# Kernel tuning notes

Measured on AMD Instinct MI355X. Metric: run time of the kernel, lower is better.

Reference implementation:

```python
import jax, jax.numpy as jnp
import numpy as np

B, S, D, H = 2, 2048, 1024, 16
HD = D // H  # head_dim = 64


def setup_inputs() -> dict:
    key = jax.random.key(0)
    ks = jax.random.split(key, 9)
    xav = float(np.sqrt(6.0 / (D + D)))  # xavier_uniform bound for square matrices
    def lin_w(k):
        return jax.random.uniform(k, (D, D), jnp.float32, -xav, xav)
    return {
        "x": jax.random.normal(ks[0], (B, S, D), jnp.float32),
        "mask": jnp.ones((B, S), jnp.int32),
        "Wq": lin_w(ks[1]), "bq": jnp.zeros((D,), jnp.float32),
        "Wk": lin_w(ks[2]), "bk": jnp.zeros((D,), jnp.float32),
        "Wv": lin_w(ks[3]), "bv": jnp.zeros((D,), jnp.float32),
        "Wo": lin_w(ks[4]), "bo": jnp.zeros((D,), jnp.float32),
    }


def reference(x, mask, Wq, bq, Wk, bk, Wv, bv, Wo, bo):
    # Linear projections (torch Linear: y = x @ W.T + b)
    q = x @ Wq.T + bq
    k = x @ Wk.T + bk
    v = x @ Wv.T + bv
    # [B, S, D] -> [B, H, S, HD]
    q = q.reshape(B, S, H, HD).transpose(0, 2, 1, 3)
    k = k.reshape(B, S, H, HD).transpose(0, 2, 1, 3)
    v = v.reshape(B, S, H, HD).transpose(0, 2, 1, 3)
    scores = jnp.einsum("bhqd,bhkd->bhqk", q, k) / jnp.sqrt(jnp.float32(HD))
    # mask [B, S] -> [B, 1, 1, S]; masked_fill where mask == 0
    m = mask[:, None, None, :]
    scores = jnp.where(m == 0, jnp.float32(-1e9), scores)
    attn = jax.nn.softmax(scores, axis=-1)
    # dropout in eval mode = identity
    out = jnp.einsum("bhqk,bhkd->bhqd", attn, v)
    out = out.transpose(0, 2, 1, 3).reshape(B, S, D)
    return out @ Wo.T + bo
```

## Files before the change

kernel.cpp:

```cpp
#include <hip/hip_runtime.h>
#include <stdint.h>

#define B_   2
#define S_   2048
#define D_   1024
#define H_   16
#define HD_  64
#define NTOK (B_ * S_)

typedef unsigned short u16;
typedef __bf16 bf16x8 __attribute__((ext_vector_type(8)));
typedef float  f32x4  __attribute__((ext_vector_type(4)));
typedef u16    u16x4  __attribute__((ext_vector_type(4)));

#define OFF_FLAG ((size_t)0)
#define OFF_BIAS ((size_t)64)
#define OFF_MB   ((size_t)32768)
#define OFF_X    ((size_t)65536)
#define SZ_X     ((size_t)NTOK * D_ * 2)
#define OFF_W    (OFF_X + SZ_X)
#define SZ_W     ((size_t)D_ * D_ * 2)
#define OFF_Q    (OFF_W + 4 * SZ_W)
#define SZ_T     SZ_X
#define OFF_K2   (OFF_Q + SZ_T)
#define OFF_VT   (OFF_K2 + SZ_T)
#define OFF_AO   (OFF_VT + SZ_T)

__device__ __forceinline__ float bf2f(u16 h) {
    union { uint32_t u; float f; } c; c.u = ((uint32_t)h) << 16; return c.f;
}
__device__ __forceinline__ u16 f2bf(float f) {
    union { float f; uint32_t u; } c; c.f = f;
    uint32_t r = c.u + 0x7fffu + ((c.u >> 16) & 1u);
    return (u16)(r >> 16);
}
__device__ __forceinline__ void glds16(const u16* g, u16* l) {
    __builtin_amdgcn_global_load_lds(
        (const __attribute__((address_space(1))) uint32_t*)g,
        (__attribute__((address_space(3))) uint32_t*)l,
        16, 0, 0);
}
__device__ __forceinline__ f32x4 mfma16(bf16x8 a, bf16x8 b, f32x4 c) {
    return __builtin_amdgcn_mfma_f32_16x16x32_bf16(a, b, c, 0, 0, 0);
}

__global__ void detect_kernel(const void* wq, char* ws) {
    __shared__ int ok;
    if (threadIdx.x == 0) ok = 1;
    __syncthreads();
    const u16* p = (const u16*)wq;
    bool bad = false;
    for (int j = 0; j < 8; ++j) {
        float v = bf2f(p[(threadIdx.x * 8 + j) * 2]);
        if (!(v > -1.0f && v < 1.0f)) bad = true;
    }
    if (bad) ok = 0;
    __syncthreads();
    if (threadIdx.x == 0) *(int*)(ws + OFF_FLAG) = ok;
}

__global__ void convert_kernel(const void* x, const void* wq, const void* wk,
                               const void* wv, const void* wo,
                               const void* bq, const void* bk, const void* bv,
                               const void* bo, const int* mask, char* ws) {
    const int is_bf16 = *(const int*)(ws + OFF_FLAG);
    u16* Xd = (u16*)(ws + OFF_X);
    u16* Wd = (u16*)(ws + OFF_W);
    float* Bd = (float*)(ws + OFF_BIAS);
    float* Mbd = (float*)(ws + OFF_MB);
    const uint32_t NX = (uint32_t)NTOK * D_;
    const uint32_t NW = (uint32_t)D_ * D_;
    const uint32_t NB = 4u * D_;
    const uint32_t total = NX + 4 * NW + NB + (uint32_t)NTOK;
    for (uint32_t i = blockIdx.x * 256u + threadIdx.x; i < total;
         i += gridDim.x * 256u) {
        if (i < NX + 4 * NW) {
            const void* src; uint32_t si; u16* dst;
            if (i < NX) { src = x; si = i; dst = Xd + i; }
            else {
                uint32_t j = i - NX;
                uint32_t w = j >> 20; si = j & (NW - 1u);
                src = (w == 0) ? wq : (w == 1) ? wk : (w == 2) ? wv : wo;
                dst = Wd + j;
            }
            *dst = is_bf16 ? ((const u16*)src)[si] : f2bf(((const float*)src)[si]);
        } else if (i < NX + 4 * NW + NB) {
            uint32_t j = i - NX - 4 * NW;
            uint32_t w = j >> 10; uint32_t si = j & (D_ - 1u);
            const void* src = (w == 0) ? bq : (w == 1) ? bk : (w == 2) ? bv : bo;
            Bd[j] = is_bf16 ? bf2f(((const u16*)src)[si]) : ((const float*)src)[si];
        } else {
            uint32_t j = i - NX - 4 * NW - NB;
            Mbd[j] = (mask[j] == 0) ? -1.0e9f : 0.0f;
        }
    }
}

__global__ void qkv_gemm(char* ws) {
    __shared__ alignas(16) u16 As[128 * 32];
    __shared__ alignas(16) u16 Bs[128 * 32];
    const int z = blockIdx.z;
    const u16* A    = (const u16*)(ws + OFF_X);
    const u16* Bt   = (const u16*)(ws + OFF_W + (size_t)z * SZ_W);
    const float* bias = (const float*)(ws + OFF_BIAS) + z * D_;
    u16* Qd  = (u16*)(ws + OFF_Q);
    u16* Kd  = (u16*)(ws + OFF_K2);
    u16* Vtd = (u16*)(ws + OFF_VT);

    const int tid = threadIdx.x, lane = tid & 63, wave = tid >> 6;
    const int wm = (wave & 1) * 64, wn = (wave >> 1) * 64;
    const int m0 = blockIdx.y * 128, n0 = blockIdx.x * 128;
    const int lr = lane & 15, quad = lane >> 4;
    const int srow = tid >> 2;
    const int scol = (((tid & 3) ^ ((tid >> 3) & 3)) * 8);
    const int rd_off = (quad ^ ((lr >> 1) & 3)) * 8;

    f32x4 acc[4][4];
#pragma unroll
    for (int i = 0; i < 4; i++)
#pragma unroll
        for (int j = 0; j < 4; j++) acc[i][j] = (f32x4){0.f, 0.f, 0.f, 0.f};

    const u16* Ag0 = A  + (size_t)(m0 + srow)      * D_ + scol;
    const u16* Ag1 = A  + (size_t)(m0 + srow + 64) * D_ + scol;
    const u16* Bg0 = Bt + (size_t)(n0 + srow)      * D_ + scol;
    const u16* Bg1 = Bt + (size_t)(n0 + srow + 64) * D_ + scol;

    for (int k0 = 0; k0 < D_; k0 += 32) {
        glds16(Ag0 + k0, &As[tid * 8]);
        glds16(Ag1 + k0, &As[2048 + tid * 8]);
        glds16(Bg0 + k0, &Bs[tid * 8]);
        glds16(Bg1 + k0, &Bs[2048 + tid * 8]);
        __syncthreads();
        bf16x8 a[4], b[4];
#pragma unroll
        for (int i = 0; i < 4; i++) a[i] = *(const bf16x8*)&As[(wm + i * 16 + lr) * 32 + rd_off];
#pragma unroll
        for (int j = 0; j < 4; j++) b[j] = *(const bf16x8*)&Bs[(wn + j * 16 + lr) * 32 + rd_off];
#pragma unroll
        for (int i = 0; i < 4; i++)
#pragma unroll
            for (int j = 0; j < 4; j++) acc[i][j] = mfma16(a[i], b[j], acc[i][j]);
        __syncthreads();
    }
#pragma unroll
    for (int i = 0; i < 4; i++) {
        const int row_b = m0 + wm + i * 16 + quad * 4;
#pragma unroll
        for (int j = 0; j < 4; j++) {
            const int col = n0 + wn + j * 16 + lr;
            const float bv_ = bias[col];
            const int h = col >> 6, hd = col & 63;
            if (z == 2) {
                const int bb = row_b >> 11, s = row_b & 2047;
                u16x4 pk;
#pragma unroll
                for (int r = 0; r < 4; r++) pk[r] = f2bf(acc[i][j][r] + bv_);
                *(u16x4*)&Vtd[(((size_t)(bb * H_ + h)) * HD_ + hd) * S_ + s] = pk;
            } else {
#pragma unroll
                for (int r = 0; r < 4; r++) {
                    const int row = row_b + r;
                    const int bb = row >> 11, s = row & 2047;
                    const float v = acc[i][j][r] + bv_;
                    const size_t idx = (((size_t)(bb * H_ + h)) * S_ + s) * HD_ + hd;
                    if (z == 0) Qd[idx] = f2bf(v * 0.125f);
                    else        Kd[idx] = f2bf(v);
                }
            }
        }
    }
}

__global__ void __launch_bounds__(128)
attn_kernel(char* ws) {
    __shared__ alignas(16) u16 Ks[64 * 64];
    __shared__ alignas(16) u16 Vts[64 * 64];
    __shared__ alignas(16) u16 Ps[2][32 * 64];

    const u16* Qb  = (const u16*)(ws + OFF_Q);
    const u16* Kb  = (const u16*)(ws + OFF_K2);
    const u16* Vtb = (const u16*)(ws + OFF_VT);
    const float* Mb = (const float*)(ws + OFF_MB);
    u16* AO = (u16*)(ws + OFF_AO);

    const int tid = threadIdx.x, lane = tid & 63, wave = tid >> 6;
    const int bh = blockIdx.y, b = bh >> 4, h = bh & 15;
    const int qb = blockIdx.x * 64 + wave * 32;
    const int lr = lane & 15, quad = lane >> 4;
    const int sx = lr & 7;

    const u16* Qbh = Qb  + (size_t)bh * S_ * HD_;
    const u16* Kbh = Kb  + (size_t)bh * S_ * HD_;
    const u16* Vbh = Vtb + (size_t)bh * HD_ * S_;
    const float* Mbb = Mb + b * S_;

    const int st_r = tid >> 3;
    const int st_c = (tid & 7) ^ (st_r & 7);

    bf16x8 qf[2][2];
#pragma unroll
    for (int s = 0; s < 2; ++s)
#pragma unroll
        for (int hf = 0; hf < 2; ++hf)
            qf[s][hf] = *(const bf16x8*)&Qbh[(size_t)(qb + s * 16 + lr) * HD_ + hf * 32 + quad * 8];

    float m_i[2] = {-1e30f, -1e30f}, l_i[2] = {0.f, 0.f};
    f32x4 oacc[2][4];
#pragma unroll
    for (int s = 0; s < 2; ++s)
#pragma unroll
        for (int j = 0; j < 4; ++j) oacc[s][j] = (f32x4){0.f, 0.f, 0.f, 0.f};

    u16* Pw = &Ps[wave][0];

    for (int kt = 0; kt < S_ / 64; ++kt) {
        const int k0 = kt * 64;
        const u16* Kt = Kbh + (size_t)(k0 + st_r) * HD_ + st_c * 8;
        const u16* Vt = Vbh + (size_t)st_r * S_ + k0 + st_c * 8;
#pragma unroll
        for (int t = 0; t < 4; ++t) {
            glds16(Kt + (size_t)t * 16 * HD_, &Ks[(tid + t * 128) * 8]);
            glds16(Vt + (size_t)t * 16 * S_,  &Vts[(tid + t * 128) * 8]);
        }
        __syncthreads();

        f32x4 sc[2][4];
#pragma unroll
        for (int j = 0; j < 4; ++j) {
            const int krow = (j * 16 + lr) * 64;
            bf16x8 kfA = *(const bf16x8*)&Ks[krow + ((quad    ) ^ sx) * 8];
            bf16x8 kfB = *(const bf16x8*)&Ks[krow + ((quad + 4) ^ sx) * 8];
            f32x4 mb = *(const f32x4*)&Mbb[k0 + j * 16 + quad * 4];
#pragma unroll
            for (int s = 0; s < 2; ++s) {
                f32x4 t0 = mfma16(kfA, qf[s][0], (f32x4){0.f, 0.f, 0.f, 0.f});
                t0 = mfma16(kfB, qf[s][1], t0);
                sc[s][j] = t0 + mb;
            }
        }
        bf16x8 vf[4][2];
#pragma unroll
        for (int j2 = 0; j2 < 4; ++j2) {
            const int vrow = (j2 * 16 + lr) * 64;
            vf[j2][0] = *(const bf16x8*)&Vts[vrow + ((quad    ) ^ sx) * 8];
            vf[j2][1] = *(const bf16x8*)&Vts[vrow + ((quad + 4) ^ sx) * 8];
        }

#pragma unroll
        for (int s = 0; s < 2; ++s) {
            float mx = -1e30f;
#pragma unroll
            for (int j = 0; j < 4; ++j)
#pragma unroll
                for (int r = 0; r < 4; ++r) mx = fmaxf(mx, sc[s][j][r]);
            mx = fmaxf(mx, __shfl_xor(mx, 16, 64));
            mx = fmaxf(mx, __shfl_xor(mx, 32, 64));
            const float mnew = fmaxf(m_i[s], mx);
            const float alpha = __expf(m_i[s] - mnew);

            const int prow = (s * 16 + lr) * 64;
            f32x4 rs4 = (f32x4){0.f, 0.f, 0.f, 0.f};
#pragma unroll
            for (int j = 0; j < 4; ++j) {
                f32x4 p;
#pragma unroll
                for (int r = 0; r < 4; ++r) p[r] = __expf(sc[s][j][r] - mnew);
                rs4 += p;
                u16x4 pk;
#pragma unroll
                for (int r = 0; r < 4; ++r) pk[r] = f2bf(p[r]);
                *(u16x4*)&Pw[prow + (((2 * j + (quad >> 1)) ^ sx) * 8) + (quad & 1) * 4] = pk;
            }
            float rs = (rs4[0] + rs4[1]) + (rs4[2] + rs4[3]);
            rs += __shfl_xor(rs, 16, 64);
            rs += __shfl_xor(rs, 32, 64);
            l_i[s] = l_i[s] * alpha + rs;
            m_i[s] = mnew;

#pragma unroll
            for (int r = 0; r < 4; ++r) {
                const float ab = __shfl(alpha, ((lane >> 4) << 2) + r, 64);
                oacc[s][0][r] *= ab; oacc[s][1][r] *= ab;
                oacc[s][2][r] *= ab; oacc[s][3][r] *= ab;
            }
            bf16x8 pf0 = *(const bf16x8*)&Pw[prow + ((quad    ) ^ sx) * 8];
            bf16x8 pf1 = *(const bf16x8*)&Pw[prow + ((quad + 4) ^ sx) * 8];
#pragma unroll
            for (int j2 = 0; j2 < 4; ++j2) {
                oacc[s][j2] = mfma16(pf0, vf[j2][0], oacc[s][j2]);
                oacc[s][j2] = mfma16(pf1, vf[j2][1], oacc[s][j2]);
            }
        }
        __syncthreads();
    }
#pragma unroll
    for (int s = 0; s < 2; ++s) {
        const float linv = 1.0f / l_i[s];
#pragma unroll
        for (int r = 0; r < 4; ++r) {
            const float lb = __shfl(linv, ((lane >> 4) << 2) + r, 64);
            const int q = qb + s * 16 + quad * 4 + r;
            u16* dst = AO + (size_t)(b * S_ + q) * D_ + h * HD_;
#pragma unroll
            for (int j2 = 0; j2 < 4; ++j2)
                dst[j2 * 16 + lr] = f2bf(oacc[s][j2][r] * lb);
        }
    }
}

__global__ void out_gemm(char* ws, void* dout) {
    __shared__ alignas(16) u16 As[128 * 32];
    __shared__ alignas(16) u16 Bs[128 * 32];
    const u16* A  = (const u16*)(ws + OFF_AO);
    const u16* Bt = (const u16*)(ws + OFF_W + 3 * SZ_W);
    const float* bias = (const float*)(ws + OFF_BIAS) + 3 * D_;
    const int out_bf16 = *(const int*)(ws + OFF_FLAG);

    const int tid = threadIdx.x, lane = tid & 63, wave = tid >> 6;
    const int wm = (wave & 1) * 64, wn = (wave >> 1) * 64;
    const int m0 = blockIdx.y * 128, n0 = blockIdx.x * 128;
    const int lr = lane & 15, quad = lane >> 4;
    const int srow = tid >> 2;
    const int scol = (((tid & 3) ^ ((tid >> 3) & 3)) * 8);
    const int rd_off = (quad ^ ((lr >> 1) & 3)) * 8;

    f32x4 acc[4][4];
#pragma unroll
    for (int i = 0; i < 4; i++)
#pragma unroll
        for (int j = 0; j < 4; j++) acc[i][j] = (f32x4){0.f, 0.f, 0.f, 0.f};

    const u16* Ag0 = A  + (size_t)(m0 + srow)      * D_ + scol;
    const u16* Ag1 = A  + (size_t)(m0 + srow + 64) * D_ + scol;
    const u16* Bg0 = Bt + (size_t)(n0 + srow)      * D_ + scol;
    const u16* Bg1 = Bt + (size_t)(n0 + srow + 64) * D_ + scol;

    for (int k0 = 0; k0 < D_; k0 += 32) {
        glds16(Ag0 + k0, &As[tid * 8]);
        glds16(Ag1 + k0, &As[2048 + tid * 8]);
        glds16(Bg0 + k0, &Bs[tid * 8]);
        glds16(Bg1 + k0, &Bs[2048 + tid * 8]);
        __syncthreads();
        bf16x8 a[4], b[4];
#pragma unroll
        for (int i = 0; i < 4; i++) a[i] = *(const bf16x8*)&As[(wm + i * 16 + lr) * 32 + rd_off];
#pragma unroll
        for (int j = 0; j < 4; j++) b[j] = *(const bf16x8*)&Bs[(wn + j * 16 + lr) * 32 + rd_off];
#pragma unroll
        for (int i = 0; i < 4; i++)
#pragma unroll
            for (int j = 0; j < 4; j++) acc[i][j] = mfma16(a[i], b[j], acc[i][j]);
        __syncthreads();
    }
#pragma unroll
    for (int i = 0; i < 4; i++) {
        const int row_b = m0 + wm + i * 16 + quad * 4;
#pragma unroll
        for (int j = 0; j < 4; j++) {
            const int col = n0 + wn + j * 16 + lr;
            const float bv_ = bias[col];
#pragma unroll
            for (int r = 0; r < 4; r++) {
                const int row = row_b + r;
                const float v = acc[i][j][r] + bv_;
                const size_t idx = (size_t)row * D_ + col;
                if (out_bf16) ((u16*)dout)[idx] = f2bf(v);
                else          ((float*)dout)[idx] = v;
            }
        }
    }
}

extern "C" void kernel_launch(void* const* d_in, const int* in_sizes, int n_in,
                              void* d_out, int out_size, void* d_ws, size_t ws_size,
                              hipStream_t stream) {
    (void)in_sizes; (void)n_in; (void)out_size; (void)ws_size;
    const void* x  = d_in[0];
    const int* mask = (const int*)d_in[1];
    const void* wq = d_in[2]; const void* bq = d_in[3];
    const void* wk = d_in[4]; const void* bk = d_in[5];
    const void* wv = d_in[6]; const void* bv = d_in[7];
    const void* wo = d_in[8]; const void* bo = d_in[9];
    char* ws = (char*)d_ws;

    detect_kernel<<<dim3(1), dim3(256), 0, stream>>>(wq, ws);
    convert_kernel<<<dim3(2048), dim3(256), 0, stream>>>(x, wq, wk, wv, wo,
                                                         bq, bk, bv, bo, mask, ws);
    qkv_gemm<<<dim3(8, 32, 3), dim3(256), 0, stream>>>(ws);
    attn_kernel<<<dim3(S_ / 64, B_ * H_), dim3(128), 0, stream>>>(ws);
    out_gemm<<<dim3(8, 32), dim3(256), 0, stream>>>(ws, d_out);
}
```

Measured before the change: 243.1 us.

## Fuse detection into convert, skip unmasked tiles, direct-load K/V in attention

Folds the dtype-detection kernel into the convert kernel to save a launch, and precomputes per-64-key-tile mask flags so attention adds the mask bias only on tiles that contain masked keys. The attention kernel becomes single-wave blocks that load K and V fragments straight from global memory into registers, dropping the shared-memory staging and its barriers. Q is pre-scaled by log2(e)/sqrt(d) so softmax can use exp2f, and P is converted to bf16 by truncation via a byte perm. The QKV GEMM swaps operands for Q and K so each lane stores four contiguous head-dim elements. The trade-off is redundant global loads of K/V per wave and slightly coarser bf16 rounding of P.

Result: slower. 292.8 us (+20.4%).

```diff
diff --git a/kernel.cpp b/kernel.cpp
--- a/kernel.cpp
+++ b/kernel.cpp
@@ -13,9 +13,12 @@
 typedef float  f32x4  __attribute__((ext_vector_type(4)));
 typedef u16    u16x4  __attribute__((ext_vector_type(4)));
 
+#define QSCALE 0.180336880f
+
 #define OFF_FLAG ((size_t)0)
 #define OFF_BIAS ((size_t)64)
 #define OFF_MB   ((size_t)32768)
+#define OFF_MF   ((size_t)49152)
 #define OFF_X    ((size_t)65536)
 #define SZ_X     ((size_t)NTOK * D_ * 2)
 #define OFF_W    (OFF_X + SZ_X)
@@ -43,36 +46,42 @@
 __device__ __forceinline__ f32x4 mfma16(bf16x8 a, bf16x8 b, f32x4 c) {
     return __builtin_amdgcn_mfma_f32_16x16x32_bf16(a, b, c, 0, 0, 0);
 }
-
-__global__ void detect_kernel(const void* wq, char* ws) {
-    __shared__ int ok;
-    if (threadIdx.x == 0) ok = 1;
-    __syncthreads();
-    const u16* p = (const u16*)wq;
-    bool bad = false;
-    for (int j = 0; j < 8; ++j) {
-        float v = bf2f(p[(threadIdx.x * 8 + j) * 2]);
-        if (!(v > -1.0f && v < 1.0f)) bad = true;
-    }
-    if (bad) ok = 0;
-    __syncthreads();
-    if (threadIdx.x == 0) *(int*)(ws + OFF_FLAG) = ok;
+__device__ __forceinline__ uint32_t pk_bf_trunc(float f0, float f1) {
+    return __builtin_amdgcn_perm(__builtin_bit_cast(uint32_t, f1),
+                                 __builtin_bit_cast(uint32_t, f0), 0x07060302u);
 }
 
 __global__ void convert_kernel(const void* x, const void* wq, const void* wk,
                                const void* wv, const void* wo,
                                const void* bq, const void* bk, const void* bv,
                                const void* bo, const int* mask, char* ws) {
-    const int is_bf16 = *(const int*)(ws + OFF_FLAG);
+    __shared__ int s_ok;
+    const int tid = threadIdx.x;
+    if (tid == 0) s_ok = 1;
+    __syncthreads();
+    {
+        const u16* p = (const u16*)wq;
+        bool bad = false;
+        for (int j = 0; j < 8; ++j) {
+            float v = bf2f(p[(tid * 8 + j) * 2]);
+            if (!(v > -1.0f && v < 1.0f)) bad = true;
+        }
+        if (bad) s_ok = 0;
+    }
+    __syncthreads();
+    const int is_bf16 = s_ok;
+    if (blockIdx.x == 0 && tid == 0) *(int*)(ws + OFF_FLAG) = is_bf16;
+
     u16* Xd = (u16*)(ws + OFF_X);
     u16* Wd = (u16*)(ws + OFF_W);
     float* Bd = (float*)(ws + OFF_BIAS);
     float* Mbd = (float*)(ws + OFF_MB);
+    int* MFd = (int*)(ws + OFF_MF);
     const uint32_t NX = (uint32_t)NTOK * D_;
     const uint32_t NW = (uint32_t)D_ * D_;
     const uint32_t NB = 4u * D_;
-    const uint32_t total = NX + 4 * NW + NB + (uint32_t)NTOK;
-    for (uint32_t i = blockIdx.x * 256u + threadIdx.x; i < total;
+    const uint32_t total = NX + 4 * NW + NB + (uint32_t)NTOK + B_ * 32;
+    for (uint32_t i = blockIdx.x * 256u + tid; i < total;
          i += gridDim.x * 256u) {
         if (i < NX + 4 * NW) {
             const void* src; uint32_t si; u16* dst;
@@ -89,9 +98,16 @@
             uint32_t w = j >> 10; uint32_t si = j & (D_ - 1u);
             const void* src = (w == 0) ? bq : (w == 1) ? bk : (w == 2) ? bv : bo;
             Bd[j] = is_bf16 ? bf2f(((const u16*)src)[si]) : ((const float*)src)[si];
-        } else {
+        } else if (i < NX + 4 * NW + NB + (uint32_t)NTOK) {
             uint32_t j = i - NX - 4 * NW - NB;
             Mbd[j] = (mask[j] == 0) ? -1.0e9f : 0.0f;
+        } else {
+            uint32_t f = i - NX - 4 * NW - NB - (uint32_t)NTOK;
+            uint32_t bb = f >> 5, kt = f & 31;
+            int any = 0;
+            for (int e = 0; e < 64; ++e)
+                any |= (mask[bb * S_ + kt * 64 + e] == 0);
+            MFd[f] = any;
         }
     }
 }
@@ -100,8 +116,8 @@
     __shared__ alignas(16) u16 As[128 * 32];
     __shared__ alignas(16) u16 Bs[128 * 32];
     const int z = blockIdx.z;
-    const u16* A    = (const u16*)(ws + OFF_X);
-    const u16* Bt   = (const u16*)(ws + OFF_W + (size_t)z * SZ_W);
+    const u16* X  = (const u16*)(ws + OFF_X);
+    const u16* W  = (const u16*)(ws + OFF_W + (size_t)z * SZ_W);
     const float* bias = (const float*)(ws + OFF_BIAS) + z * D_;
     u16* Qd  = (u16*)(ws + OFF_Q);
     u16* Kd  = (u16*)(ws + OFF_K2);
@@ -109,22 +125,25 @@
 
     const int tid = threadIdx.x, lane = tid & 63, wave = tid >> 6;
     const int wm = (wave & 1) * 64, wn = (wave >> 1) * 64;
-    const int m0 = blockIdx.y * 128, n0 = blockIdx.x * 128;
     const int lr = lane & 15, quad = lane >> 4;
     const int srow = tid >> 2;
     const int scol = (((tid & 3) ^ ((tid >> 3) & 3)) * 8);
     const int rd_off = (quad ^ ((lr >> 1) & 3)) * 8;
 
+    const u16* Araw; const u16* Braw; int m0, n0;
+    if (z < 2) { Araw = W; Braw = X; m0 = blockIdx.x * 128; n0 = blockIdx.y * 128; }
+    else       { Araw = X; Braw = W; m0 = blockIdx.y * 128; n0 = blockIdx.x * 128; }
+
     f32x4 acc[4][4];
 #pragma unroll
     for (int i = 0; i < 4; i++)
 #pragma unroll
         for (int j = 0; j < 4; j++) acc[i][j] = (f32x4){0.f, 0.f, 0.f, 0.f};
 
-    const u16* Ag0 = A  + (size_t)(m0 + srow)      * D_ + scol;
-    const u16* Ag1 = A  + (size_t)(m0 + srow + 64) * D_ + scol;
-    const u16* Bg0 = Bt + (size_t)(n0 + srow)      * D_ + scol;
-    const u16* Bg1 = Bt + (size_t)(n0 + srow + 64) * D_ + scol;
+    const u16* Ag0 = Araw + (size_t)(m0 + srow)      * D_ + scol;
+    const u16* Ag1 = Araw + (size_t)(m0 + srow + 64) * D_ + scol;
+    const u16* Bg0 = Braw + (size_t)(n0 + srow)      * D_ + scol;
+    const u16* Bg1 = Braw + (size_t)(n0 + srow + 64) * D_ + scol;
 
     for (int k0 = 0; k0 < D_; k0 += 32) {
         glds16(Ag0 + k0, &As[tid * 8]);
@@ -143,50 +162,58 @@
             for (int j = 0; j < 4; j++) acc[i][j] = mfma16(a[i], b[j], acc[i][j]);
         __syncthreads();
     }
-#pragma unroll
-    for (int i = 0; i < 4; i++) {
-        const int row_b = m0 + wm + i * 16 + quad * 4;
-#pragma unroll
-        for (int j = 0; j < 4; j++) {
-            const int col = n0 + wn + j * 16 + lr;
-            const float bv_ = bias[col];
-            const int h = col >> 6, hd = col & 63;
-            if (z == 2) {
-                const int bb = row_b >> 11, s = row_b & 2047;
+
+    if (z < 2) {
+        u16* dst0 = (z == 0) ? Qd : Kd;
+        const float sc_ = (z == 0) ? QSCALE : 1.0f;
+#pragma unroll
+        for (int i = 0; i < 4; i++) {
+            const int fb = m0 + wm + i * 16 + quad * 4;
+            const f32x4 b4 = *(const f32x4*)&bias[fb];
+            const int h = fb >> 6, hd0 = fb & 63;
+#pragma unroll
+            for (int j = 0; j < 4; j++) {
+                const int tok = n0 + wn + j * 16 + lr;
+                const int bb = tok >> 11, s = tok & 2047;
                 u16x4 pk;
 #pragma unroll
+                for (int r = 0; r < 4; r++) pk[r] = f2bf((acc[i][j][r] + b4[r]) * sc_);
+                *(u16x4*)&dst0[(((size_t)(bb * H_ + h)) * S_ + s) * HD_ + hd0] = pk;
+            }
+        }
+    } else {
+#pragma unroll
+        for (int i = 0; i < 4; i++) {
+            const int row_b = m0 + wm + i * 16 + quad * 4;
+            const int bb = row_b >> 11, s0 = row_b & 2047;
+#pragma unroll
+            for (int j = 0; j < 4; j++) {
+                const int col = n0 + wn + j * 16 + lr;
+                const float bv_ = bias[col];
+                const int h = col >> 6, hd = col & 63;
+                u16x4 pk;
+#pragma unroll
                 for (int r = 0; r < 4; r++) pk[r] = f2bf(acc[i][j][r] + bv_);
-                *(u16x4*)&Vtd[(((size_t)(bb * H_ + h)) * HD_ + hd) * S_ + s] = pk;
-            } else {
-#pragma unroll
-                for (int r = 0; r < 4; r++) {
-                    const int row = row_b + r;
-                    const int bb = row >> 11, s = row & 2047;
-                    const float v = acc[i][j][r] + bv_;
-                    const size_t idx = (((size_t)(bb * H_ + h)) * S_ + s) * HD_ + hd;
-                    if (z == 0) Qd[idx] = f2bf(v * 0.125f);
-                    else        Kd[idx] = f2bf(v);
-                }
-            }
-        }
-    }
-}
-
-__global__ void __launch_bounds__(128)
+                *(u16x4*)&Vtd[(((size_t)(bb * H_ + h)) * HD_ + hd) * S_ + s0] = pk;
+            }
+        }
+    }
+}
+
+__global__ void __launch_bounds__(64)
 attn_kernel(char* ws) {
-    __shared__ alignas(16) u16 Ks[64 * 64];
-    __shared__ alignas(16) u16 Vts[64 * 64];
-    __shared__ alignas(16) u16 Ps[2][32 * 64];
+    __shared__ alignas(16) u16 Pw[32 * 64];
 
     const u16* Qb  = (const u16*)(ws + OFF_Q);
     const u16* Kb  = (const u16*)(ws + OFF_K2);
     const u16* Vtb = (const u16*)(ws + OFF_VT);
     const float* Mb = (const float*)(ws + OFF_MB);
+    const int* MF = (const int*)(ws + OFF_MF);
     u16* AO = (u16*)(ws + OFF_AO);
 
-    const int tid = threadIdx.x, lane = tid & 63, wave = tid >> 6;
+    const int lane = threadIdx.x;
     const int bh = blockIdx.y, b = bh >> 4, h = bh & 15;
-    const int qb = blockIdx.x * 64 + wave * 32;
+    const int qb = blockIdx.x * 32;
     const int lr = lane & 15, quad = lane >> 4;
     const int sx = lr & 7;
 
@@ -194,9 +221,7 @@
     const u16* Kbh = Kb  + (size_t)bh * S_ * HD_;
     const u16* Vbh = Vtb + (size_t)bh * HD_ * S_;
     const float* Mbb = Mb + b * S_;
-
-    const int st_r = tid >> 3;
-    const int st_c = (tid & 7) ^ (st_r & 7);
+    const int* MFb = MF + b * 32;
 
     bf16x8 qf[2][2];
 #pragma unroll
@@ -212,39 +237,34 @@
 #pragma unroll
         for (int j = 0; j < 4; ++j) oacc[s][j] = (f32x4){0.f, 0.f, 0.f, 0.f};
 
-    u16* Pw = &Ps[wave][0];
-
     for (int kt = 0; kt < S_ / 64; ++kt) {
         const int k0 = kt * 64;
-        const u16* Kt = Kbh + (size_t)(k0 + st_r) * HD_ + st_c * 8;
-        const u16* Vt = Vbh + (size_t)st_r * S_ + k0 + st_c * 8;
-#pragma unroll
-        for (int t = 0; t < 4; ++t) {
-            glds16(Kt + (size_t)t * 16 * HD_, &Ks[(tid + t * 128) * 8]);
-            glds16(Vt + (size_t)t * 16 * S_,  &Vts[(tid + t * 128) * 8]);
-        }
-        __syncthreads();
+        const u16* Kp = Kbh + (size_t)(k0 + lr) * HD_ + quad * 8;
+        const u16* Vp = Vbh + (size_t)lr * S_ + k0 + quad * 8;
+        bf16x8 kA[4], kB[4], vA[4], vB[4];
+#pragma unroll
+        for (int j = 0; j < 4; ++j) {
+            kA[j] = *(const bf16x8*)(Kp + j * 16 * HD_);
+            kB[j] = *(const bf16x8*)(Kp + j * 16 * HD_ + 32);
+            vA[j] = *(const bf16x8*)(Vp + (size_t)j * 16 * S_);
+            vB[j] = *(const bf16x8*)(Vp + (size_t)j * 16 * S_ + 32);
+        }
 
         f32x4 sc[2][4];
 #pragma unroll
-        for (int j = 0; j < 4; ++j) {
-            const int krow = (j * 16 + lr) * 64;
-            bf16x8 kfA = *(const bf16x8*)&Ks[krow + ((quad    ) ^ sx) * 8];
-            bf16x8 kfB = *(const bf16x8*)&Ks[krow + ((quad + 4) ^ sx) * 8];
-            f32x4 mb = *(const f32x4*)&Mbb[k0 + j * 16 + quad * 4];
+        for (int j = 0; j < 4; ++j)
 #pragma unroll
             for (int s = 0; s < 2; ++s) {
-                f32x4 t0 = mfma16(kfA, qf[s][0], (f32x4){0.f, 0.f, 0.f, 0.f});
-                t0 = mfma16(kfB, qf[s][1], t0);
-                sc[s][j] = t0 + mb;
-            }
-        }
-        bf16x8 vf[4][2];
-#pragma unroll
-        for (int j2 = 0; j2 < 4; ++j2) {
-            const int vrow = (j2 * 16 + lr) * 64;
-            vf[j2][0] = *(const bf16x8*)&Vts[vrow + ((quad    ) ^ sx) * 8];
-            vf[j2][1] = *(const bf16x8*)&Vts[vrow + ((quad + 4) ^ sx) * 8];
+                f32x4 t0 = mfma16(kA[j], qf[s][0], (f32x4){0.f, 0.f, 0.f, 0.f});
+                sc[s][j] = mfma16(kB[j], qf[s][1], t0);
+            }
+        if (MFb[kt]) {
+#pragma unroll
+            for (int j = 0; j < 4; ++j) {
+                const f32x4 mb = *(const f32x4*)&Mbb[k0 + j * 16 + quad * 4];
+#pragma unroll
+                for (int s = 0; s < 2; ++s) sc[s][j] += mb;
+            }
         }
 
 #pragma unroll
@@ -257,7 +277,7 @@
             mx = fmaxf(mx, __shfl_xor(mx, 16, 64));
             mx = fmaxf(mx, __shfl_xor(mx, 32, 64));
             const float mnew = fmaxf(m_i[s], mx);
-            const float alpha = __expf(m_i[s] - mnew);
+            const float alpha = exp2f(m_i[s] - mnew);
 
             const int prow = (s * 16 + lr) * 64;
             f32x4 rs4 = (f32x4){0.f, 0.f, 0.f, 0.f};
@@ -265,12 +285,12 @@
             for (int j = 0; j < 4; ++j) {
                 f32x4 p;
 #pragma unroll
-                for (int r = 0; r < 4; ++r) p[r] = __expf(sc[s][j][r] - mnew);
+                for (int r = 0; r < 4; ++r) p[r] = exp2f(sc[s][j][r] - mnew);
                 rs4 += p;
-                u16x4 pk;
-#pragma unroll
-                for (int r = 0; r < 4; ++r) pk[r] = f2bf(p[r]);
-                *(u16x4*)&Pw[prow + (((2 * j + (quad >> 1)) ^ sx) * 8) + (quad & 1) * 4] = pk;
+                uint2 pk;
+                pk.x = pk_bf_trunc(p[0], p[1]);
+                pk.y = pk_bf_trunc(p[2], p[3]);
+                *(uint2*)&Pw[prow + (((2 * j + (quad >> 1)) ^ sx) * 8) + (quad & 1) * 4] = pk;
             }
             float rs = (rs4[0] + rs4[1]) + (rs4[2] + rs4[3]);
             rs += __shfl_xor(rs, 16, 64);
@@ -280,7 +300,7 @@
 
 #pragma unroll
             for (int r = 0; r < 4; ++r) {
-                const float ab = __shfl(alpha, ((lane >> 4) << 2) + r, 64);
+                const float ab = __shfl(alpha, (quad << 2) + r, 64);
                 oacc[s][0][r] *= ab; oacc[s][1][r] *= ab;
                 oacc[s][2][r] *= ab; oacc[s][3][r] *= ab;
             }
@@ -288,18 +308,17 @@
             bf16x8 pf1 = *(const bf16x8*)&Pw[prow + ((quad + 4) ^ sx) * 8];
 #pragma unroll
             for (int j2 = 0; j2 < 4; ++j2) {
-                oacc[s][j2] = mfma16(pf0, vf[j2][0], oacc[s][j2]);
-                oacc[s][j2] = mfma16(pf1, vf[j2][1], oacc[s][j2]);
-            }
-        }
-        __syncthreads();
+                oacc[s][j2] = mfma16(pf0, vA[j2], oacc[s][j2]);
+                oacc[s][j2] = mfma16(pf1, vB[j2], oacc[s][j2]);
+            }
+        }
     }
 #pragma unroll
     for (int s = 0; s < 2; ++s) {
         const float linv = 1.0f / l_i[s];
 #pragma unroll
         for (int r = 0; r < 4; ++r) {
-            const float lb = __shfl(linv, ((lane >> 4) << 2) + r, 64);
+            const float lb = __shfl(linv, (quad << 2) + r, 64);
             const int q = qb + s * 16 + quad * 4 + r;
             u16* dst = AO + (size_t)(b * S_ + q) * D_ + h * HD_;
 #pragma unroll
@@ -384,10 +403,9 @@
     const void* wo = d_in[8]; const void* bo = d_in[9];
     char* ws = (char*)d_ws;
 
-    detect_kernel<<<dim3(1), dim3(256), 0, stream>>>(wq, ws);
     convert_kernel<<<dim3(2048), dim3(256), 0, stream>>>(x, wq, wk, wv, wo,
                                                          bq, bk, bv, bo, mask, ws);
     qkv_gemm<<<dim3(8, 32, 3), dim3(256), 0, stream>>>(ws);
-    attn_kernel<<<dim3(S_ / 64, B_ * H_), dim3(128), 0, stream>>>(ws);
+    attn_kernel<<<dim3(S_ / 32, B_ * H_), dim3(64), 0, stream>>>(ws);
     out_gemm<<<dim3(8, 32), dim3(256), 0, stream>>>(ws, d_out);
 }
```
